# Kernel optimization log

Hardware: AMD Instinct MI355X
Metric: run time of the kernel (lower is better)

## Reference

```python
import jax, jax.numpy as jnp
import numpy as np

B = 4        # number of point clouds (equal-sized, batch ids are sorted blocks)
K = 3        # knn_interpolate k
EPS_D = 1e-16
EPS_BN = 1e-5


def setup_inputs() -> dict:
    key = jax.random.key(0)
    ks = jax.random.split(key, 12)
    N_src, N_tgt = 2048, 8192
    C, C_skip = 256, 128
    x = jax.random.normal(ks[0], (B * N_src, C), dtype=jnp.float32)
    pos = jax.random.normal(ks[1], (B * N_src, 3), dtype=jnp.float32)
    x_skip = jax.random.normal(ks[2], (B * N_tgt, C_skip), dtype=jnp.float32)
    pos_skip = jax.random.normal(ks[3], (B * N_tgt, 3), dtype=jnp.float32)
    batch = jnp.repeat(jnp.arange(B, dtype=jnp.int64), N_src)
    batch_skip = jnp.repeat(jnp.arange(B, dtype=jnp.int64), N_tgt)
    d_in = C + C_skip  # 384
    W1 = jax.random.normal(ks[4], (d_in, 256), dtype=jnp.float32) / np.sqrt(d_in)
    b1 = jnp.zeros((256,), dtype=jnp.float32)
    g1 = jnp.ones((256,), dtype=jnp.float32)
    be1 = jnp.zeros((256,), dtype=jnp.float32)
    W2 = jax.random.normal(ks[5], (256, 256), dtype=jnp.float32) / 16.0
    b2 = jnp.zeros((256,), dtype=jnp.float32)
    g2 = jnp.ones((256,), dtype=jnp.float32)
    be2 = jnp.zeros((256,), dtype=jnp.float32)
    return dict(x=x, pos=pos, batch=batch, x_skip=x_skip, pos_skip=pos_skip,
                batch_skip=batch_skip, W1=W1, b1=b1, g1=g1, be1=be1,
                W2=W2, b2=b2, g2=g2, be2=be2)


def _knn_interpolate(x, pos, pos_skip):
    # equal-size clouds: reshape instead of per-batch masking
    C = x.shape[1]
    N = pos.shape[0] // B
    M = pos_skip.shape[0] // B
    ps = pos.reshape(B, N, 3)
    pt = pos_skip.reshape(B, M, 3)
    # squared distances [B, M, N] via |a|^2 + |b|^2 - 2ab
    d2 = (jnp.sum(pt * pt, -1)[:, :, None]
          + jnp.sum(ps * ps, -1)[:, None, :]
          - 2.0 * jnp.einsum('bmd,bnd->bmn', pt, ps))
    neg_d2, idx = jax.lax.top_k(-d2, K)            # idx: [B, M, K]
    w = 1.0 / jnp.maximum(-neg_d2, EPS_D)          # inverse squared distance
    xf = x.reshape(B, N, C)
    feats = xf[jnp.arange(B)[:, None, None], idx]  # [B, M, K, C] irregular gather
    y = jnp.sum(feats * w[..., None], axis=2) / jnp.sum(w, axis=2)[..., None]
    return y.reshape(B * M, C)


def _mlp_block(h, W, b, g, be):
    h = jnp.maximum(h @ W + b, 0.0)                # Linear + ReLU
    mu = jnp.mean(h, axis=0)
    var = jnp.mean((h - mu) ** 2, axis=0)          # biased var (torch BN training)
    return g * (h - mu) / jnp.sqrt(var + EPS_BN) + be


def reference(x, pos, batch, x_skip, pos_skip, batch_skip,
              W1, b1, g1, be1, W2, b2, g2, be2):
    y = _knn_interpolate(x, pos, pos_skip)
    h = jnp.concatenate([y, x_skip], axis=1)       # [B*M, 384]
    h = _mlp_block(h, W1, b1, g1, be1)
    h = _mlp_block(h, W2, b2, g2, be2)
    return h
```

## Files before the change

### kernel.cpp

```cpp
#include <hip/hip_runtime.h>
#include <hip/hip_bf16.h>

typedef __attribute__((ext_vector_type(8))) short short8;
typedef __attribute__((ext_vector_type(4))) int   i32x4;
typedef __attribute__((ext_vector_type(4))) float f32x4;
typedef __attribute__((ext_vector_type(2))) float f32x2;
typedef __attribute__((ext_vector_type(8))) float f32x8;

constexpr int BATCH  = 4;
constexpr int NSRC   = 2048;
constexpr int NTGT   = 8192;
constexpr int C_IN   = 256;
constexpr int C_SKIP = 128;
constexpr int DIN    = 384;
constexpr int HID    = 256;
constexpr int MROWS  = BATCH * NTGT;

constexpr int TGT_PER_BLK = 16;
constexpr int KNN_BLOCKS  = MROWS / TGT_PER_BLK;
constexpr int WT_BLOCKS   = 8;
constexpr int LDS_STRIDE  = 36;

__device__ __forceinline__ short f2bf(float v) {
    __hip_bfloat16 h = __float2bfloat16(v);
    return (short)__builtin_bit_cast(unsigned short, h);
}
__device__ __forceinline__ float bf2f(short s) {
    return __uint_as_float(((unsigned)(unsigned short)s) << 16);
}

__global__ __launch_bounds__(512, 2) void knn_kernel(const float* __restrict__ pos,
                                                     const float* __restrict__ pos_skip,
                                                     const float* __restrict__ W1,
                                                     __hip_bfloat16* __restrict__ W1T,
                                                     i32x4* __restrict__ idxo,
                                                     f32x4* __restrict__ wqo,
                                                     float* __restrict__ stats) {
#pragma clang fp contract(off)
    const int blk = blockIdx.x;
    if (blk >= KNN_BLOCKS) {
        const int e = blk - KNN_BLOCKS;
        if (e < WT_BLOCKS) {
            const int r  = e * 32 + (threadIdx.x >> 4);
            const int c0 = threadIdx.x & 15;
#pragma unroll
            for (int k = 0; k < DIN / 16; ++k) {
                int c = c0 + k * 16;
                W1T[(size_t)r * DIN + c] = __float2bfloat16(W1[(size_t)c * HID + r]);
            }
        } else {
            for (int i = threadIdx.x; i < 4 * HID; i += 512) stats[i] = 0.0f;
        }
        return;
    }
    __shared__ float4 sp[NSRC];
    const int t0 = blk * TGT_PER_BLK;
    const int b  = t0 / NTGT;
    const float* ps = pos + (size_t)b * NSRC * 3;
    for (int j = threadIdx.x; j < NSRC; j += 512) {
        float X = ps[j * 3 + 0], Y = ps[j * 3 + 1], Z = ps[j * 3 + 2];
        float s2 = ((X * X) + (Y * Y)) + (Z * Z);
        sp[j] = make_float4(X, Y, Z, s2);
    }
    __syncthreads();
    const int g  = threadIdx.x >> 5;
    const int s  = threadIdx.x & 31;
    const int tr = t0 + g;
    const float px = pos_skip[tr * 3 + 0], py = pos_skip[tr * 3 + 1], pz = pos_skip[tr * 3 + 2];
    const float pt2 = ((px * px) + (py * py)) + (pz * pz);
    const f32x2 px2 = {px, px}, py2 = {py, py}, pz2 = {pz, pz}, ptv = {pt2, pt2};
    const f32x2 two = {2.0f, 2.0f};

    float dreg[64];
    float a0 = 3e38f, a1 = 3e38f, a2 = 3e38f;
#pragma unroll
    for (int k = 0; k < NSRC / 64; ++k) {
        const int j1 = k * 64 + s;
        const int j2 = j1 + 32;
        float4 sa = sp[j1];
        float4 sb = sp[j2];
        f32x2 vx = {sa.x, sb.x}, vy = {sa.y, sb.y}, vz = {sa.z, sb.z}, vw = {sa.w, sb.w};
        f32x2 dot = ((px2 * vx) + (py2 * vy)) + (pz2 * vz);
        f32x2 d2v = (ptv + vw) - (two * dot);
        dreg[2 * k]     = d2v.x;
        dreg[2 * k + 1] = d2v.y;
#pragma unroll
        for (int h = 0; h < 2; ++h) {
            float d = h == 0 ? d2v.x : d2v.y;
            float n0 = fminf(a0, d);
            float n1 = __builtin_amdgcn_fmed3f(a0, a1, d);
            float n2 = fminf(a2, fmaxf(a1, d));
            a0 = n0; a1 = n1; a2 = n2;
        }
    }
#pragma unroll
    for (int m = 1; m <= 16; m <<= 1) {
        float oa = __shfl_xor(a0, m), ob = __shfl_xor(a1, m), oc = __shfl_xor(a2, m);
        float minb = fminf(a1, ob);
        float maxa = fmaxf(a0, oa);
        float maxb = fmaxf(a1, ob);
        float minc = fminf(a2, oc);
        float n0 = fminf(a0, oa);
        float n1 = __builtin_amdgcn_fmed3f(a0, oa, minb);
        float n2 = __builtin_amdgcn_fmed3f(minb, maxa, fminf(maxb, minc));
        a0 = n0; a1 = n1; a2 = n2;
    }

    float bd0 = 3e38f, bd1 = 3e38f, bd2 = 3e38f;
    int   bi0 = 0x7fffffff, bi1 = 0x7fffffff, bi2 = 0x7fffffff;
#pragma unroll
    for (int i = 0; i < 64; ++i) {
        float d2 = dreg[i];
        if (__any(d2 <= a2)) {
            const int j = (i >> 1) * 64 + ((i & 1) << 5) + s;
            bool c0 = d2 < bd0, c1 = d2 < bd1, c2 = d2 < bd2;
            bd2 = c1 ? bd1 : (c2 ? d2 : bd2);  bi2 = c1 ? bi1 : (c2 ? j : bi2);
            bd1 = c0 ? bd0 : (c1 ? d2 : bd1);  bi1 = c0 ? bi0 : (c1 ? j : bi1);
            bd0 = c0 ? d2  : bd0;              bi0 = c0 ? j  : bi0;
        }
    }
#pragma unroll
    for (int m = 1; m <= 16; m <<= 1) {
        float od0 = __shfl_xor(bd0, m), od1 = __shfl_xor(bd1, m), od2 = __shfl_xor(bd2, m);
        int   oi0 = __shfl_xor(bi0, m), oi1 = __shfl_xor(bi1, m), oi2 = __shfl_xor(bi2, m);
#pragma unroll
        for (int e = 0; e < 3; ++e) {
            float d = e == 0 ? od0 : (e == 1 ? od1 : od2);
            int   i = e == 0 ? oi0 : (e == 1 ? oi1 : oi2);
            bool c0 = (d < bd0) || (d == bd0 && i < bi0);
            bool c1 = (d < bd1) || (d == bd1 && i < bi1);
            bool c2 = (d < bd2) || (d == bd2 && i < bi2);
            bd2 = c1 ? bd1 : (c2 ? d : bd2);  bi2 = c1 ? bi1 : (c2 ? i : bi2);
            bd1 = c0 ? bd0 : (c1 ? d : bd1);  bi1 = c0 ? bi0 : (c1 ? i : bi1);
            bd0 = c0 ? d   : bd0;             bi0 = c0 ? i  : bi0;
        }
    }
    if (s == 0) {
        float w0 = 1.0f / fmaxf(bd0, 1e-16f);
        float w1 = 1.0f / fmaxf(bd1, 1e-16f);
        float w2 = 1.0f / fmaxf(bd2, 1e-16f);
        float inv = 1.0f / ((w0 + w1) + w2);
        idxo[tr] = i32x4{bi0, bi1, bi2, 0};
        wqo[tr]  = f32x4{w0 * inv, w1 * inv, w2 * inv, 0.0f};
    }
}

__global__ __launch_bounds__(256, 1) void zs_kernel(const float* __restrict__ x,
                                                    const float* __restrict__ xs,
                                                    const __hip_bfloat16* __restrict__ W1T,
                                                    __hip_bfloat16* __restrict__ Z,
                                                    __hip_bfloat16* __restrict__ S) {
    __shared__ short As[128 * LDS_STRIDE];
    const int blk = blockIdx.x;
    const float* A;
    __hip_bfloat16* out;
    int K, koff, m0;
    if (blk < 64) { A = x;  out = Z; K = 256; koff = 0;   m0 = blk * 128; }
    else          { A = xs; out = S; K = 128; koff = 256; m0 = (blk - 64) * 128; }
    const int t = threadIdx.x;
    const int wid = t >> 6, lane = t & 63;
    const int wr = wid & 1, wcq = wid >> 1;
    const int l15 = lane & 15, l4 = lane >> 4;
    const int arow = t >> 1, ac16 = (t & 1) * 16;
    const short* Wsh = (const short*)W1T;
    f32x4 acc[4][8] = {};
    for (int kt = 0; kt < K / 32; ++kt) {
        const float* src = A + (size_t)(m0 + arow) * K + kt * 32 + ac16;
        float4 f0 = *(const float4*)(src);
        float4 f1 = *(const float4*)(src + 4);
        float4 f2 = *(const float4*)(src + 8);
        float4 f3 = *(const float4*)(src + 12);
        short8 s0 = {f2bf(f0.x), f2bf(f0.y), f2bf(f0.z), f2bf(f0.w),
                     f2bf(f1.x), f2bf(f1.y), f2bf(f1.z), f2bf(f1.w)};
        short8 s1 = {f2bf(f2.x), f2bf(f2.y), f2bf(f2.z), f2bf(f2.w),
                     f2bf(f3.x), f2bf(f3.y), f2bf(f3.z), f2bf(f3.w)};
        __syncthreads();
        *(short8*)(&As[arow * LDS_STRIDE + ac16])     = s0;
        *(short8*)(&As[arow * LDS_STRIDE + ac16 + 8]) = s1;
        __syncthreads();
        short8 af[4], bfr[8];
#pragma unroll
        for (int mi = 0; mi < 4; ++mi)
            af[mi] = *(const short8*)(&As[(wr * 64 + mi * 16 + l15) * LDS_STRIDE + l4 * 8]);
#pragma unroll
        for (int ni = 0; ni < 8; ++ni)
            bfr[ni] = *(const short8*)(Wsh + (size_t)(wcq * 128 + ni * 16 + l15) * DIN + koff + kt * 32 + l4 * 8);
#pragma unroll
        for (int mi = 0; mi < 4; ++mi)
#pragma unroll
            for (int ni = 0; ni < 8; ++ni)
                acc[mi][ni] = __builtin_amdgcn_mfma_f32_16x16x32_bf16(af[mi], bfr[ni], acc[mi][ni], 0, 0, 0);
    }
#pragma unroll
    for (int mi = 0; mi < 4; ++mi)
#pragma unroll
        for (int r = 0; r < 4; ++r) {
            int rowg = m0 + wr * 64 + mi * 16 + l4 * 4 + r;
#pragma unroll
            for (int ni = 0; ni < 8; ++ni) {
                int col = wcq * 128 + ni * 16 + l15;
                out[(size_t)rowg * HID + col] = __float2bfloat16(acc[mi][ni][r]);
            }
        }
}

__global__ __launch_bounds__(256) void interp_kernel(const __hip_bfloat16* __restrict__ Z,
                                                     const __hip_bfloat16* __restrict__ S,
                                                     const i32x4* __restrict__ idxo,
                                                     const f32x4* __restrict__ wqo,
                                                     const float* __restrict__ b1,
                                                     __hip_bfloat16* __restrict__ H1) {
    const int t = blockIdx.x * 256 + threadIdx.x;
    const int r = t >> 5;
    const int c = (t & 31) * 8;
    i32x4 id = idxo[r];
    f32x4 wq = wqo[r];
    const int zb = (r >> 13) << 11;
    const short* Zs = (const short*)Z;
    short8 z0 = *(const short8*)(Zs + (size_t)(zb + id.x) * HID + c);
    short8 z1 = *(const short8*)(Zs + (size_t)(zb + id.y) * HID + c);
    short8 z2 = *(const short8*)(Zs + (size_t)(zb + id.z) * HID + c);
    short8 sv = *(const short8*)((const short*)S + (size_t)r * HID + c);
    f32x4 b0 = *(const f32x4*)(b1 + c);
    f32x4 b4 = *(const f32x4*)(b1 + c + 4);
    short8 ho;
#pragma unroll
    for (int e = 0; e < 8; ++e) {
        float bb = e < 4 ? b0[e & 3] : b4[e & 3];
        float v = wq.x * bf2f(z0[e]) + wq.y * bf2f(z1[e]) + wq.z * bf2f(z2[e])
                  + bf2f(sv[e]) + bb;
        ho[e] = f2bf(fmaxf(v, 0.0f));
    }
    *(short8*)((short*)H1 + (size_t)r * HID + c) = ho;
}

__global__ __launch_bounds__(256) void stats1_kernel(const __hip_bfloat16* __restrict__ H1,
                                                     float* __restrict__ sum1,
                                                     float* __restrict__ sq1) {
    const int c  = threadIdx.x;
    const int r0 = blockIdx.x * (MROWS / 128);
    const short* Hs = (const short*)H1;
    float s = 0.0f, q = 0.0f;
#pragma unroll 8
    for (int r = 0; r < MROWS / 128; ++r) {
        float v = bf2f(Hs[(size_t)(r0 + r) * HID + c]);
        s += v;
        q += v * v;
    }
    atomicAdd(&sum1[c], s);
    atomicAdd(&sq1[c], q);
}

template <int K>
__global__ __launch_bounds__(256, 1) void gemm_kernel(const __hip_bfloat16* __restrict__ A,
                                                      const __hip_bfloat16* __restrict__ WT,
                                                      const float* __restrict__ bias,
                                                      __hip_bfloat16* __restrict__ outp,
                                                      float* __restrict__ colsum,
                                                      float* __restrict__ colsq) {
    __shared__ short As[128 * LDS_STRIDE];
    const int t = threadIdx.x;
    const int m0 = blockIdx.x * 128;
    const int wid = t >> 6, lane = t & 63;
    const int wr = wid & 1, wcq = wid >> 1;
    const int l15 = lane & 15, l4 = lane >> 4;
    const int arow = t >> 1, acol8 = (t & 1) * 8;
    f32x4 acc[4][8] = {};
    const short* Ash = (const short*)A;
    const short* Wsh = (const short*)WT;
    for (int kt = 0; kt < K / 32; ++kt) {
        short8 v0 = *(const short8*)(Ash + (size_t)(m0 + arow) * K + kt * 32 + acol8);
        short8 v1 = *(const short8*)(Ash + (size_t)(m0 + arow) * K + kt * 32 + acol8 + 16);
        __syncthreads();
        *(short8*)(&As[arow * LDS_STRIDE + acol8]) = v0;
        *(short8*)(&As[arow * LDS_STRIDE + acol8 + 16]) = v1;
        __syncthreads();
        short8 af[4], bfr[8];
#pragma unroll
        for (int mi = 0; mi < 4; ++mi)
            af[mi] = *(const short8*)(&As[(wr * 64 + mi * 16 + l15) * LDS_STRIDE + l4 * 8]);
#pragma unroll
        for (int ni = 0; ni < 8; ++ni)
            bfr[ni] = *(const short8*)(Wsh + (size_t)(wcq * 128 + ni * 16 + l15) * K + kt * 32 + l4 * 8);
#pragma unroll
        for (int mi = 0; mi < 4; ++mi)
#pragma unroll
            for (int ni = 0; ni < 8; ++ni)
                acc[mi][ni] = __builtin_amdgcn_mfma_f32_16x16x32_bf16(af[mi], bfr[ni], acc[mi][ni], 0, 0, 0);
    }
    float bv[8];
    int col[8];
#pragma unroll
    for (int ni = 0; ni < 8; ++ni) {
        col[ni] = wcq * 128 + ni * 16 + l15;
        bv[ni] = bias[col[ni]];
    }
    float csum[8] = {}, csq[8] = {};
#pragma unroll
    for (int mi = 0; mi < 4; ++mi) {
#pragma unroll
        for (int r = 0; r < 4; ++r) {
            int rowg = m0 + wr * 64 + mi * 16 + l4 * 4 + r;
#pragma unroll
            for (int ni = 0; ni < 8; ++ni) {
                float v = fmaxf(acc[mi][ni][r] + bv[ni], 0.0f);
                outp[(size_t)rowg * HID + col[ni]] = __float2bfloat16(v);
                csum[ni] += v;
                csq[ni] += v * v;
            }
        }
    }
#pragma unroll
    for (int ni = 0; ni < 8; ++ni) {
        float sv = csum[ni], q = csq[ni];
        sv += __shfl_xor(sv, 16); sv += __shfl_xor(sv, 32);
        q  += __shfl_xor(q, 16);  q  += __shfl_xor(q, 32);
        if (l4 == 0) {
            atomicAdd(&colsum[col[ni]], sv);
            atomicAdd(&colsq[col[ni]], q);
        }
    }
}

__global__ __launch_bounds__(256) void foldw2_kernel(const float* __restrict__ W2,
                                                     const float* __restrict__ b2,
                                                     const float* __restrict__ sum1,
                                                     const float* __restrict__ sq1,
                                                     const float* __restrict__ g1,
                                                     const float* __restrict__ be1,
                                                     __hip_bfloat16* __restrict__ W2T,
                                                     float* __restrict__ bias2f) {
    __shared__ float red[256];
    const int n = blockIdx.x, k = threadIdx.x;
    float mu  = sum1[k] * (1.0f / MROWS);
    float var = sq1[k] * (1.0f / MROWS) - mu * mu;
    float scv = g1[k] / sqrtf(var + 1e-5f);
    float shv = be1[k] - mu * scv;
    float v = W2[(size_t)k * HID + n];
    W2T[(size_t)n * HID + k] = __float2bfloat16(scv * v);
    red[k] = shv * v;
    __syncthreads();
    for (int s = 128; s > 0; s >>= 1) {
        if (k < s) red[k] += red[k + s];
        __syncthreads();
    }
    if (k == 0) bias2f[n] = b2[n] + red[0];
}

__global__ __launch_bounds__(256) void bn2_kernel(const __hip_bfloat16* __restrict__ h2,
                                                  const float* __restrict__ sum2,
                                                  const float* __restrict__ sq2,
                                                  const float* __restrict__ g2,
                                                  const float* __restrict__ be2,
                                                  float* __restrict__ out) {
    __shared__ float lsc[HID], lsh[HID];
    {
        int c = threadIdx.x;
        float mu  = sum2[c] * (1.0f / MROWS);
        float var = sq2[c] * (1.0f / MROWS) - mu * mu;
        float scv = g2[c] / sqrtf(var + 1e-5f);
        lsc[c] = scv;
        lsh[c] = be2[c] - mu * scv;
    }
    __syncthreads();
    int idx = blockIdx.x * blockDim.x + threadIdx.x;
    const int total = MROWS * HID / 8;
    for (; idx < total; idx += gridDim.x * blockDim.x) {
        short8 v = *(const short8*)(h2 + (size_t)idx * 8);
        int c = (idx * 8) & (HID - 1);
        f32x8 o;
#pragma unroll
        for (int e = 0; e < 8; ++e) {
            float f = bf2f(v[e]);
            o[e] = lsc[c + e] * f + lsh[c + e];
        }
        *(f32x8*)(out + (size_t)idx * 8) = o;
    }
}

extern "C" void kernel_launch(void* const* d_in, const int* in_sizes, int n_in,
                              void* d_out, int out_size, void* d_ws, size_t ws_size,
                              hipStream_t stream) {
    const float* x    = (const float*)d_in[0];
    const float* pos  = (const float*)d_in[1];
    const float* xs   = (const float*)d_in[3];
    const float* poss = (const float*)d_in[4];
    const float* W1   = (const float*)d_in[6];
    const float* b1   = (const float*)d_in[7];
    const float* g1   = (const float*)d_in[8];
    const float* be1  = (const float*)d_in[9];
    const float* W2   = (const float*)d_in[10];
    const float* b2   = (const float*)d_in[11];
    const float* g2   = (const float*)d_in[12];
    const float* be2  = (const float*)d_in[13];

    char* ws = (char*)d_ws;
    size_t off = 0;
    auto alloc = [&](size_t bytes) -> void* {
        void* p = ws + off;
        off += (bytes + 255) & ~(size_t)255;
        return p;
    };
    __hip_bfloat16* W1T   = (__hip_bfloat16*)alloc((size_t)HID * DIN * 2);
    __hip_bfloat16* W2T   = (__hip_bfloat16*)alloc((size_t)HID * HID * 2);
    float*          stats = (float*)alloc(4 * HID * sizeof(float));
    float *sum1 = stats, *sq1 = stats + HID, *sum2 = stats + 2 * HID, *sq2 = stats + 3 * HID;
    float*          bias2f = (float*)alloc(HID * sizeof(float));
    i32x4*          idxo  = (i32x4*)alloc((size_t)MROWS * 16);
    f32x4*          wqo   = (f32x4*)alloc((size_t)MROWS * 16);
    __hip_bfloat16* Z     = (__hip_bfloat16*)alloc((size_t)BATCH * NSRC * HID * 2);
    __hip_bfloat16* S     = (__hip_bfloat16*)alloc((size_t)MROWS * HID * 2);
    __hip_bfloat16* H1    = (__hip_bfloat16*)alloc((size_t)MROWS * HID * 2);
    __hip_bfloat16* H2    = S;

    knn_kernel<<<KNN_BLOCKS + WT_BLOCKS + 1, 512, 0, stream>>>(pos, poss, W1, W1T, idxo, wqo, stats);
    zs_kernel<<<64 + MROWS / 128, 256, 0, stream>>>(x, xs, W1T, Z, S);
    interp_kernel<<<MROWS * 32 / 256, 256, 0, stream>>>(Z, S, idxo, wqo, b1, H1);
    stats1_kernel<<<128, 256, 0, stream>>>(H1, sum1, sq1);
    foldw2_kernel<<<HID, 256, 0, stream>>>(W2, b2, sum1, sq1, g1, be1, W2T, bias2f);
    gemm_kernel<HID><<<MROWS / 128, 256, 0, stream>>>(H1, W2T, bias2f, H2, sum2, sq2);
    bn2_kernel<<<1024, 256, 0, stream>>>(H2, sum2, sq2, g2, be2, (float*)d_out);
}
```

Baseline: 134.7 us.

## Recompute KNN distances instead of caching 64 registers, raise occupancy bound

Drops the 64-entry per-thread distance register array and recomputes distances from LDS in the second (index-tracking) pass. The first-pass top-3 threshold is split into two independent chains (even/odd halves) that merge at the end, shortening the dependency chain. Launch bounds go from 2 to 8 blocks per CU to force lower register use and higher occupancy. The cost is a second pass of LDS reads and FMAs, and possible spilling under the tighter register cap.

```diff
diff --git a/kernel.cpp b/kernel.cpp
--- a/kernel.cpp
+++ b/kernel.cpp
@@ -29,7 +29,7 @@
     return __uint_as_float(((unsigned)(unsigned short)s) << 16);
 }
 
-__global__ __launch_bounds__(512, 2) void knn_kernel(const float* __restrict__ pos,
+__global__ __launch_bounds__(512, 8) void knn_kernel(const float* __restrict__ pos,
                                                      const float* __restrict__ pos_skip,
                                                      const float* __restrict__ W1,
                                                      __hip_bfloat16* __restrict__ W1T,
@@ -71,8 +71,8 @@
     const f32x2 px2 = {px, px}, py2 = {py, py}, pz2 = {pz, pz}, ptv = {pt2, pt2};
     const f32x2 two = {2.0f, 2.0f};
 
-    float dreg[64];
-    float a0 = 3e38f, a1 = 3e38f, a2 = 3e38f;
+    float a0 = 3e38f, a1 = 3e38f, a2v = 3e38f;
+    float b0 = 3e38f, b1 = 3e38f, b2v = 3e38f;
 #pragma unroll
     for (int k = 0; k < NSRC / 64; ++k) {
         const int j1 = k * 64 + s;
@@ -82,41 +82,66 @@
         f32x2 vx = {sa.x, sb.x}, vy = {sa.y, sb.y}, vz = {sa.z, sb.z}, vw = {sa.w, sb.w};
         f32x2 dot = ((px2 * vx) + (py2 * vy)) + (pz2 * vz);
         f32x2 d2v = (ptv + vw) - (two * dot);
-        dreg[2 * k]     = d2v.x;
-        dreg[2 * k + 1] = d2v.y;
-#pragma unroll
-        for (int h = 0; h < 2; ++h) {
-            float d = h == 0 ? d2v.x : d2v.y;
+        {
+            float d = d2v.x;
             float n0 = fminf(a0, d);
             float n1 = __builtin_amdgcn_fmed3f(a0, a1, d);
-            float n2 = fminf(a2, fmaxf(a1, d));
-            a0 = n0; a1 = n1; a2 = n2;
-        }
+            float n2 = fminf(a2v, fmaxf(a1, d));
+            a0 = n0; a1 = n1; a2v = n2;
+        }
+        {
+            float d = d2v.y;
+            float n0 = fminf(b0, d);
+            float n1 = __builtin_amdgcn_fmed3f(b0, b1, d);
+            float n2 = fminf(b2v, fmaxf(b1, d));
+            b0 = n0; b1 = n1; b2v = n2;
+        }
+    }
+    {
+        float minb = fminf(a1, b1);
+        float maxa = fmaxf(a0, b0);
+        float maxb = fmaxf(a1, b1);
+        float minc = fminf(a2v, b2v);
+        float n0 = fminf(a0, b0);
+        float n1 = __builtin_amdgcn_fmed3f(a0, b0, minb);
+        float n2 = __builtin_amdgcn_fmed3f(minb, maxa, fminf(maxb, minc));
+        a0 = n0; a1 = n1; a2v = n2;
     }
 #pragma unroll
     for (int m = 1; m <= 16; m <<= 1) {
-        float oa = __shfl_xor(a0, m), ob = __shfl_xor(a1, m), oc = __shfl_xor(a2, m);
+        float oa = __shfl_xor(a0, m), ob = __shfl_xor(a1, m), oc = __shfl_xor(a2v, m);
         float minb = fminf(a1, ob);
         float maxa = fmaxf(a0, oa);
         float maxb = fmaxf(a1, ob);
-        float minc = fminf(a2, oc);
+        float minc = fminf(a2v, oc);
         float n0 = fminf(a0, oa);
         float n1 = __builtin_amdgcn_fmed3f(a0, oa, minb);
         float n2 = __builtin_amdgcn_fmed3f(minb, maxa, fminf(maxb, minc));
-        a0 = n0; a1 = n1; a2 = n2;
-    }
+        a0 = n0; a1 = n1; a2v = n2;
+    }
+    const float cut = a2v;
 
     float bd0 = 3e38f, bd1 = 3e38f, bd2 = 3e38f;
     int   bi0 = 0x7fffffff, bi1 = 0x7fffffff, bi2 = 0x7fffffff;
 #pragma unroll
-    for (int i = 0; i < 64; ++i) {
-        float d2 = dreg[i];
-        if (__any(d2 <= a2)) {
-            const int j = (i >> 1) * 64 + ((i & 1) << 5) + s;
-            bool c0 = d2 < bd0, c1 = d2 < bd1, c2 = d2 < bd2;
-            bd2 = c1 ? bd1 : (c2 ? d2 : bd2);  bi2 = c1 ? bi1 : (c2 ? j : bi2);
-            bd1 = c0 ? bd0 : (c1 ? d2 : bd1);  bi1 = c0 ? bi0 : (c1 ? j : bi1);
-            bd0 = c0 ? d2  : bd0;              bi0 = c0 ? j  : bi0;
+    for (int k = 0; k < NSRC / 64; ++k) {
+        const int j1 = k * 64 + s;
+        const int j2 = j1 + 32;
+        float4 sa = sp[j1];
+        float4 sb = sp[j2];
+        f32x2 vx = {sa.x, sb.x}, vy = {sa.y, sb.y}, vz = {sa.z, sb.z}, vw = {sa.w, sb.w};
+        f32x2 dot = ((px2 * vx) + (py2 * vy)) + (pz2 * vz);
+        f32x2 d2v = (ptv + vw) - (two * dot);
+        if (__any(d2v.x <= cut) || __any(d2v.y <= cut)) {
+#pragma unroll
+            for (int h = 0; h < 2; ++h) {
+                float d2 = h == 0 ? d2v.x : d2v.y;
+                int   j  = h == 0 ? j1 : j2;
+                bool c0 = d2 < bd0, c1 = d2 < bd1, c2 = d2 < bd2;
+                bd2 = c1 ? bd1 : (c2 ? d2 : bd2);  bi2 = c1 ? bi1 : (c2 ? j : bi2);
+                bd1 = c0 ? bd0 : (c1 ? d2 : bd1);  bi1 = c0 ? bi0 : (c1 ? j : bi1);
+                bd0 = c0 ? d2  : bd0;              bi0 = c0 ? j  : bi0;
+            }
         }
     }
 #pragma unroll
```

New measurement: 144.6 us. 7.4% more time.
